# Kernel optimization log

Hardware: AMD Instinct MI355X
Metric: run time of the kernel (lower is better)

Reference implementation:

```python
import jax, jax.numpy as jnp
import numpy as np

BITS = 32
HDC_DIM = 512
IN_SCALE = 23  # 1 + 2*input_window_size, window=11


def setup_inputs() -> dict:
    key = jax.random.key(0)
    k1, k2, k3, k4 = jax.random.split(key, 4)
    B = 2
    D = IN_SCALE * IN_SCALE  # 529
    num_nonzero = int(0.5 * D * HDC_DIM)  # 135424
    return {
        "data_input": jax.random.normal(k1, (B, 4 * IN_SCALE, IN_SCALE), dtype=jnp.float32),
        "structure_input": jax.random.normal(k2, (B, IN_SCALE, IN_SCALE), dtype=jnp.float32),
        "parameters_temp": jax.random.uniform(k3, (IN_SCALE, IN_SCALE), dtype=jnp.float32),
        "non_zero_indices": jax.random.randint(k4, (num_nonzero,), 0, D * HDC_DIM, dtype=jnp.int32),
    }


def _bit_unpack(x_float):
    # view float32 bits as int32, unpack into 0/1 per bit (little-endian bit order),
    # matching torch: x.unsqueeze(-1).bitwise_and(2**arange(bits)).ne(0)
    xi = jax.lax.bitcast_convert_type(x_float, jnp.int32)
    mask = jnp.left_shift(jnp.int32(1), jnp.arange(BITS, dtype=jnp.int32))  # [32], incl. sign bit
    return ((xi[..., None] & mask) != 0).astype(jnp.int32)  # [..., 32]


def reference(data_input, structure_input, parameters_temp, non_zero_indices):
    B = data_input.shape[0]
    n = IN_SCALE
    # channel slices
    r = data_input[:, 0:n, :].reshape(B, -1)            # [B, D]
    g = data_input[:, n:2 * n, :].reshape(B, -1)
    b = data_input[:, 2 * n:3 * n, :].reshape(B, -1)
    a = data_input[:, 3 * n:4 * n, :].reshape(B, -1)
    s = (structure_input * parameters_temp).reshape(B, -1)  # [B, D]
    D = r.shape[1]

    # sparse random scatter into flat projection buffer (faithful to torch semantics:
    # view(-1)[idx] = 1, then view(-1)[~idx] = 0 where ~idx indexes total-1-idx via negative wrap)
    total = B * D * BITS * HDC_DIM
    proj = jnp.zeros((total,), dtype=jnp.int32)
    proj = proj.at[non_zero_indices].set(1)
    proj = proj.at[total - 1 - non_zero_indices].set(0)
    proj = proj.reshape(B, D, BITS, HDC_DIM)

    # bit-unpack + broadcast-XOR against projection (no materialized repeat)
    r_bin = _bit_unpack(r)[..., None] ^ proj  # [B, D, 32, hdc]
    g_bin = _bit_unpack(g)[..., None] ^ proj
    b_bin = _bit_unpack(b)[..., None] ^ proj
    a_bin = _bit_unpack(a)[..., None] ^ proj
    s_bin = _bit_unpack(s)[..., None] ^ proj

    return (r, g, b, a, s, r_bin, g_bin, b_bin, a_bin, s_bin)
```

## Files before the change

kernel.cpp:

```cpp
#include <hip/hip_runtime.h>
#include <stdint.h>

#define IN_SCALE 23
#define DDIM 529
#define BATCH 2
#define BITS 32
#define HDC 512
#define ROW (BITS * HDC)
#define NNZ_REGION (DDIM * HDC)
#define SMALL (5 * BATCH * DDIM)
#define BIN_PER_OUT (BATCH * DDIM * ROW)
#define BIN_PER_B   (DDIM * ROW)

__global__ void scatter_mask(const int* __restrict__ idx, int n,
                             uint8_t* __restrict__ mask) {
    int i = blockIdx.x * blockDim.x + threadIdx.x;
    if (i < n) {
        int p = idx[i];
        if ((unsigned)p < NNZ_REGION) mask[p] = 1;
    }
}

__global__ __launch_bounds__(256) void bins_kernel(const float* __restrict__ data,
                                                   const float* __restrict__ structure,
                                                   const float* __restrict__ params,
                                                   const uint8_t* __restrict__ mask,
                                                   float* __restrict__ out) {
    int blk = blockIdx.x;
    int c   = blk / (BATCH * DDIM);
    int rem = blk % (BATCH * DDIM);
    int bb  = rem / DDIM;
    int d   = rem % DDIM;

    float v;
    if (c < 4) {
        v = data[bb * (4 * DDIM) + c * DDIM + d];
    } else {
        v = structure[bb * DDIM + d] * params[d];
    }
    const int x = __float_as_int(v);

    const bool useMask = (bb == 0);
    const int  dbase   = d * ROW;
    long long base = (long long)SMALL + (long long)c * BIN_PER_OUT
                   + (long long)bb * BIN_PER_B + (long long)d * ROW;
    float* o = out + base;

    int t = threadIdx.x;
    if (t == 0) {
        out[blk] = v;
        int b0 = x & 1, v0 = b0, v1 = b0;
        if (useMask && dbase < NNZ_REGION) { v0 ^= mask[dbase]; v1 ^= mask[dbase + 1]; }
        *(float2*)o = make_float2((float)v0, (float)v1);
    } else if (t == 1) {
        int b31 = (x >> 31) & 1, v0 = b31, v1 = b31;
        int p = dbase + ROW - 2;
        if (useMask && p < NNZ_REGION) { v0 ^= mask[p]; v1 ^= mask[p + 1]; }
        *(float2*)(o + ROW - 2) = make_float2((float)v0, (float)v1);
    }

    float4* om = (float4*)(o + 2);
    #pragma unroll
    for (int k = 0; k < 16; ++k) {
        int q = t + k * 256;
        if (q < 4095) {
            int e0 = 2 + q * 4;
            float4 w;
            float* wp = (float*)&w;
            #pragma unroll
            for (int u = 0; u < 4; ++u) {
                int e  = e0 + u;
                int bv = (x >> (e >> 9)) & 1;
                int p  = dbase + e;
                if (useMask && p < NNZ_REGION) bv ^= mask[p];
                wp[u] = (float)bv;
            }
            om[q] = w;
        }
    }
}

extern "C" void kernel_launch(void* const* d_in, const int* in_sizes, int n_in,
                              void* d_out, int out_size, void* d_ws, size_t ws_size,
                              hipStream_t stream) {
    const float* data      = (const float*)d_in[0];
    const float* structure = (const float*)d_in[1];
    const float* params    = (const float*)d_in[2];
    const int*   nzi       = (const int*)d_in[3];
    int nnz = in_sizes[3];

    float*   out  = (float*)d_out;
    uint8_t* mask = (uint8_t*)d_ws;

    hipMemsetAsync(mask, 0, NNZ_REGION, stream);
    scatter_mask<<<(nnz + 255) / 256, 256, 0, stream>>>(nzi, nnz, mask);
    bins_kernel<<<SMALL, 256, 0, stream>>>(data, structure, params, mask, out);
}
```

Measured before the change: 86.10 us.

## Write pure bit pattern first, then patch scattered projection ones in a fixup kernel

Drops the byte-mask memset and scatter pass along with the per-element mask reads in the big output kernel. The main kernel now writes only the broadcast sign-bit pattern, using shift-based bit extraction and nontemporal vector stores. A second kernel then walks the nonzero indices and overwrites the flipped entries in all five outputs. This trades a dense mask lookup for scattered writes after the bulk stores, and correctness depends on the fixup running after the pattern kernel in the same stream.

```diff
diff --git a/kernel.cpp b/kernel.cpp
--- a/kernel.cpp
+++ b/kernel.cpp
@@ -12,20 +12,12 @@
 #define BIN_PER_OUT (BATCH * DDIM * ROW)
 #define BIN_PER_B   (DDIM * ROW)
 
-__global__ void scatter_mask(const int* __restrict__ idx, int n,
-                             uint8_t* __restrict__ mask) {
-    int i = blockIdx.x * blockDim.x + threadIdx.x;
-    if (i < n) {
-        int p = idx[i];
-        if ((unsigned)p < NNZ_REGION) mask[p] = 1;
-    }
-}
+typedef float f32x4 __attribute__((ext_vector_type(4)));
 
-__global__ __launch_bounds__(256) void bins_kernel(const float* __restrict__ data,
-                                                   const float* __restrict__ structure,
-                                                   const float* __restrict__ params,
-                                                   const uint8_t* __restrict__ mask,
-                                                   float* __restrict__ out) {
+__global__ __launch_bounds__(256) void bins_pattern(const float* __restrict__ data,
+                                                    const float* __restrict__ structure,
+                                                    const float* __restrict__ params,
+                                                    float* __restrict__ out) {
     int blk = blockIdx.x;
     int c   = blk / (BATCH * DDIM);
     int rem = blk % (BATCH * DDIM);
@@ -38,45 +30,57 @@
     } else {
         v = structure[bb * DDIM + d] * params[d];
     }
-    const int x = __float_as_int(v);
+    const unsigned x = (unsigned)__float_as_int(v);
 
-    const bool useMask = (bb == 0);
-    const int  dbase   = d * ROW;
     long long base = (long long)SMALL + (long long)c * BIN_PER_OUT
                    + (long long)bb * BIN_PER_B + (long long)d * ROW;
     float* o = out + base;
 
-    int t = threadIdx.x;
+    const int t = threadIdx.x;
     if (t == 0) {
         out[blk] = v;
-        int b0 = x & 1, v0 = b0, v1 = b0;
-        if (useMask && dbase < NNZ_REGION) { v0 ^= mask[dbase]; v1 ^= mask[dbase + 1]; }
-        *(float2*)o = make_float2((float)v0, (float)v1);
+        float f0 = (float)(x & 1u);
+        *(float2*)o = make_float2(f0, f0);
     } else if (t == 1) {
-        int b31 = (x >> 31) & 1, v0 = b31, v1 = b31;
-        int p = dbase + ROW - 2;
-        if (useMask && p < NNZ_REGION) { v0 ^= mask[p]; v1 ^= mask[p + 1]; }
-        *(float2*)(o + ROW - 2) = make_float2((float)v0, (float)v1);
+        float f31 = (float)((x >> 31) & 1u);
+        *(float2*)(o + ROW - 2) = make_float2(f31, f31);
     }
 
-    float4* om = (float4*)(o + 2);
+    f32x4* om = (f32x4*)(o + 2);
+    const int e0     = 4 * t + 2;
+    const int jbase  = e0 >> 9;
+    const int cross  = ((e0 & 511) == 510) ? 1 : 0;
+    unsigned xs = x >> jbase;
     #pragma unroll
     for (int k = 0; k < 16; ++k) {
-        int q = t + k * 256;
+        int q = t + (k << 8);
         if (q < 4095) {
-            int e0 = 2 + q * 4;
-            float4 w;
-            float* wp = (float*)&w;
-            #pragma unroll
-            for (int u = 0; u < 4; ++u) {
-                int e  = e0 + u;
-                int bv = (x >> (e >> 9)) & 1;
-                int p  = dbase + e;
-                if (useMask && p < NNZ_REGION) bv ^= mask[p];
-                wp[u] = (float)bv;
-            }
-            om[q] = w;
+            float fa = (float)(xs & 1u);
+            float fb = (float)((xs >> cross) & 1u);
+            f32x4 w = {fa, fa, fb, fb};
+            __builtin_nontemporal_store(w, &om[q]);
         }
+        xs >>= 2;
+    }
+}
+
+__global__ __launch_bounds__(256) void bins_fixup(const int* __restrict__ idx, int n,
+                                                  const float* __restrict__ data,
+                                                  const float* __restrict__ structure,
+                                                  const float* __restrict__ params,
+                                                  float* __restrict__ out) {
+    int i = blockIdx.x * blockDim.x + threadIdx.x;
+    if (i >= n) return;
+    unsigned p = (unsigned)idx[i];
+    if (p >= NNZ_REGION) return;
+    int d = p >> 14;
+    int j = (p >> 9) & 31;
+    #pragma unroll
+    for (int c = 0; c < 5; ++c) {
+        float v = (c < 4) ? data[c * DDIM + d]
+                          : structure[d] * params[d];
+        unsigned bit = ((unsigned)__float_as_int(v) >> j) & 1u;
+        out[(long long)SMALL + (long long)c * BIN_PER_OUT + p] = (float)(bit ^ 1u);
     }
 }
 
@@ -89,10 +93,8 @@
     const int*   nzi       = (const int*)d_in[3];
     int nnz = in_sizes[3];
 
-    float*   out  = (float*)d_out;
-    uint8_t* mask = (uint8_t*)d_ws;
+    float* out = (float*)d_out;
 
-    hipMemsetAsync(mask, 0, NNZ_REGION, stream);
-    scatter_mask<<<(nnz + 255) / 256, 256, 0, stream>>>(nzi, nnz, mask);
-    bins_kernel<<<SMALL, 256, 0, stream>>>(data, structure, params, mask, out);
+    bins_pattern<<<SMALL, 256, 0, stream>>>(data, structure, params, out);
+    bins_fixup<<<(nnz + 255) / 256, 256, 0, stream>>>(nzi, nnz, data, structure, params, out);
 }
```

Result: slower. 106.8 us (+24.0%).
